# Optimization experiments

Measured on AMD Instinct MI355X. Metric: run time of the kernel, lower is better.

The kernel has to match this reference:

```python
import jax, jax.numpy as jnp
import numpy as np
import math

B, C, H, W = 16, 512, 32, 32
GROUPS = 32
EPS = 1e-5


def group_norm(x, w, b):
    # x: [B, C, H, W]; normalize within each of GROUPS channel groups over (C//G, H, W)
    Bx, Cx, Hx, Wx = x.shape
    xg = x.reshape(Bx, GROUPS, Cx // GROUPS, Hx, Wx)
    mean = xg.mean(axis=(2, 3, 4), keepdims=True)
    var = xg.var(axis=(2, 3, 4), keepdims=True)
    xg = (xg - mean) * jax.lax.rsqrt(var + EPS)
    xn = xg.reshape(Bx, Cx, Hx, Wx)
    return xn * w[None, :, None, None] + b[None, :, None, None]


def setup_inputs() -> dict:
    key = jax.random.key(0)
    ks = jax.random.split(key, 4)
    x = jax.random.normal(ks[0], (B, C, H, W), dtype=jnp.float32)
    gn_w = jnp.ones((C,), dtype=jnp.float32)
    gn_b = jnp.zeros((C,), dtype=jnp.float32)
    # Conv2d 1x1 weights as [out, in] matrices; PyTorch default init scale
    qkv_w = jax.random.normal(ks[1], (3 * C, C), dtype=jnp.float32) * (1.0 / math.sqrt(C))
    qkv_b = jnp.zeros((3 * C,), dtype=jnp.float32)
    out_w = jax.random.normal(ks[2], (C, C), dtype=jnp.float32) * (1.0 / math.sqrt(C))
    out_b = jnp.zeros((C,), dtype=jnp.float32)
    return {"x": x, "gn_w": gn_w, "gn_b": gn_b, "qkv_w": qkv_w,
            "qkv_b": qkv_b, "out_w": out_w, "out_b": out_b}


def reference(x, gn_w, gn_b, qkv_w, qkv_b, out_w, out_b):
    Bx, Cx, Hx, Wx = x.shape
    N = Hx * Wx
    h = group_norm(x, gn_w, gn_b)                       # [B, C, H, W]
    hf = h.reshape(Bx, Cx, N)                           # [B, C, N]
    # 1x1 conv == channel matmul
    qkv = jnp.einsum('oc,bcn->bon', qkv_w, hf) + qkv_b[None, :, None]  # [B, 3C, N]
    q, k, v = jnp.split(qkv, 3, axis=1)                 # each [B, C, N]
    q = q.transpose(0, 2, 1)                            # [B, N, C]
    v = v.transpose(0, 2, 1)                            # [B, N, C]
    scale = 1.0 / math.sqrt(Cx)
    attn = jnp.einsum('bnc,bcm->bnm', q, k) * scale     # [B, N, N]
    attn = jax.nn.softmax(attn, axis=-1)
    o = jnp.einsum('bnm,bmc->bnc', attn, v)             # [B, N, C]
    o = o.transpose(0, 2, 1)                            # [B, C, N]
    o = jnp.einsum('oc,bcn->bon', out_w, o) + out_b[None, :, None]
    return x + o.reshape(Bx, Cx, Hx, Wx)
```

## Files before the change

kernel.cpp:

```cpp
#include <hip/hip_runtime.h>

typedef unsigned short u16;
typedef short short8 __attribute__((ext_vector_type(8)));
typedef float floatx4 __attribute__((ext_vector_type(4)));
typedef u16 u16x4 __attribute__((ext_vector_type(4)));
typedef u16 u16x8 __attribute__((ext_vector_type(8)));

#define DEVI __device__ __forceinline__

DEVI u16 f2bf(float x) {
    union { float f; unsigned u; } c; c.f = x;
    unsigned u = c.u;
    u += 0x7fffu + ((u >> 16) & 1u);
    return (u16)(u >> 16);
}
DEVI float bf2f(u16 h) {
    union { unsigned u; float f; } c; c.u = ((unsigned)h) << 16;
    return c.f;
}

DEVI void gload_lds16(const void* g, void* l) {
    auto gp = (const __attribute__((address_space(1))) unsigned*)(unsigned long long)g;
    auto lp = (__attribute__((address_space(3))) unsigned*)(unsigned)(unsigned long long)l;
    __builtin_amdgcn_global_load_lds(gp, lp, 16, 0, 0);
}

__global__ __launch_bounds__(256) void gn_fused_kernel(const float* __restrict__ x,
                                                       const float* __restrict__ w,
                                                       const float* __restrict__ bb,
                                                       u16* __restrict__ h) {
    const int bg = blockIdx.x;
    const int b = bg >> 5, g = bg & 31;
    const float* xg = x + (long long)bg * 16384;
    const int n0 = threadIdx.x * 4;

    float4 xv[16];
    float s = 0.f, s2 = 0.f;
    #pragma unroll
    for (int cc = 0; cc < 16; cc++) {
        xv[cc] = *(const float4*)&xg[cc * 1024 + n0];
        s  += xv[cc].x + xv[cc].y + xv[cc].z + xv[cc].w;
        s2 += xv[cc].x*xv[cc].x + xv[cc].y*xv[cc].y + xv[cc].z*xv[cc].z + xv[cc].w*xv[cc].w;
    }
    #pragma unroll
    for (int m = 1; m < 64; m <<= 1) { s += __shfl_xor(s, m, 64); s2 += __shfl_xor(s2, m, 64); }
    __shared__ float rs[4], rq[4];
    if ((threadIdx.x & 63) == 0) { rs[threadIdx.x >> 6] = s; rq[threadIdx.x >> 6] = s2; }
    __syncthreads();
    float mean = (rs[0] + rs[1] + rs[2] + rs[3]) * (1.f / 16384.f);
    float var  = (rq[0] + rq[1] + rq[2] + rq[3]) * (1.f / 16384.f) - mean * mean;
    float rstd = rsqrtf(var + 1e-5f);

    u16x8 o[4][2];
    #pragma unroll
    for (int cc = 0; cc < 16; cc++) {
        int c = g * 16 + cc;
        float sc = w[c] * rstd;
        float sh = bb[c] - mean * sc;
        o[0][cc >> 3][cc & 7] = f2bf(xv[cc].x * sc + sh);
        o[1][cc >> 3][cc & 7] = f2bf(xv[cc].y * sc + sh);
        o[2][cc >> 3][cc & 7] = f2bf(xv[cc].z * sc + sh);
        o[3][cc >> 3][cc & 7] = f2bf(xv[cc].w * sc + sh);
    }
    u16* hb = h + ((long long)b * 1024 + n0) * 512 + g * 16;
    #pragma unroll
    for (int k = 0; k < 4; k++) {
        *(u16x8*)&hb[(long long)k * 512]     = o[k][0];
        *(u16x8*)&hb[(long long)k * 512 + 8] = o[k][1];
    }
}

__global__ __launch_bounds__(256) void wconv_kernel(const float* __restrict__ w1, u16* __restrict__ o1,
                                                    const float* __restrict__ w2, u16* __restrict__ o2) {
    int i = blockIdx.x * 256 + threadIdx.x;
    const float* src; u16* dst; int j;
    if (i < 196608) { src = w1; dst = o1; j = i; }
    else            { src = w2; dst = o2; j = i - 196608; }
    float4 v = *(const float4*)&src[j * 4];
    u16x4 p; p[0] = f2bf(v.x); p[1] = f2bf(v.y); p[2] = f2bf(v.z); p[3] = f2bf(v.w);
    *(u16x4*)&dst[j * 4] = p;
}

__global__ __launch_bounds__(256) void lreduce_kernel(const float* __restrict__ ps,
                                                      float* __restrict__ invl) {
    int i = blockIdx.x * 256 + threadIdx.x;
    int z = i >> 10, n = i & 1023;
    float l = 0.f;
    #pragma unroll
    for (int kb = 0; kb < 4; kb++) l += ps[((z * 4 + kb) << 10) + n];
    invl[i] = 1.f / l;
}

#define VMCNT(N) do { asm volatile("s_waitcnt vmcnt(" #N ")" ::: "memory"); \
                      __builtin_amdgcn_sched_barrier(0); } while (0)

template <bool EXPSTATS, bool AFFINE>
__global__ __launch_bounds__(512, 2)
void gemm256_kernel(const u16* __restrict__ A, const u16* __restrict__ Bt,
                    u16* __restrict__ C, float* __restrict__ aux,
                    float scale, int lda, int ldb, int ldc,
                    long long sA, long long sB, long long sC, int K) {
    int bx, by, bz;
    if (AFFINE) {
        const int lid = blockIdx.x;
        const int slot = lid >> 3;
        bz = (lid & 7) + 8 * (slot >> 4);
        const int w = slot & 15;
        bx = w & 3; by = w >> 2;
    } else { bx = blockIdx.x; by = blockIdx.y; bz = 0; }

    const int t    = threadIdx.x;
    const int lane = t & 63;
    const int wave = t >> 6;
    const int wm   = wave >> 2;
    const int wn   = wave & 3;
    const int quad = lane >> 4, lrow = lane & 15;
    const int m0 = by * 256, n0 = bx * 256;

    __shared__ __align__(16) u16 smem[65536];

    const int NT = K >> 6;

    floatx4 acc[8][4];
    #pragma unroll
    for (int i = 0; i < 8; i++)
        #pragma unroll
        for (int j = 0; j < 4; j++)
            #pragma unroll
            for (int r = 0; r < 4; r++) acc[i][j][r] = 0.f;

    const int srow = t >> 3;
    const int koff = ((t & 7) * 8) ^ (((t >> 5) & 1) << 4);
    const u16* Ab = A  + (long long)bz * sA + (long long)(m0 + srow) * lda + koff;
    const u16* Bb = Bt + (long long)bz * sB + (long long)(n0 + srow) * ldb + koff;

#define STGA(BUF, HALF, KT) do { \
    const u16* gs_ = Ab + (long long)((HALF) * 128) * lda + (KT) * 64; \
    gload_lds16(gs_,                          smem + ((BUF)*2 + (HALF)) * 8192 + t * 8); \
    gload_lds16(gs_ + (long long)64 * lda,    smem + ((BUF)*2 + (HALF)) * 8192 + 4096 + t * 8); \
} while (0)
#define STGB(BUF, HALF, KT) do { \
    const u16* gs_ = Bb + (long long)((HALF) * 128) * ldb + (KT) * 64; \
    gload_lds16(gs_,                          smem + 32768 + ((BUF)*2 + (HALF)) * 8192 + t * 8); \
    gload_lds16(gs_ + (long long)64 * ldb,    smem + 32768 + ((BUF)*2 + (HALF)) * 8192 + 4096 + t * 8); \
} while (0)

    const int swz  = ((lrow >> 2) & 1) << 4;
    const int arow = wm * 64 + lrow;
    const int brow = wn * 32 + lrow;
#define AIDX(BUF, QA, i, kk) (((BUF)*2 + (QA)) * 8192 + ((((arow + (i)*16) << 6) + (kk)*32 + (quad << 3)) ^ swz))
#define BIDX(BUF, QB, j, kk) (32768 + ((BUF)*2 + (QB)) * 8192 + ((((brow + (j)*16) << 6) + (kk)*32 + (quad << 3)) ^ swz))

#define PHASE(BUF, QA, QB, STG_STMT) do { \
    short8 paf[4][2], pbf[2][2]; \
    _Pragma("unroll") for (int i = 0; i < 4; ++i) { \
        paf[i][0] = *(const short8*)&smem[AIDX(BUF, QA, i, 0)]; \
        paf[i][1] = *(const short8*)&smem[AIDX(BUF, QA, i, 1)]; } \
    _Pragma("unroll") for (int j = 0; j < 2; ++j) { \
        pbf[j][0] = *(const short8*)&smem[BIDX(BUF, QB, j, 0)]; \
        pbf[j][1] = *(const short8*)&smem[BIDX(BUF, QB, j, 1)]; } \
    STG_STMT; \
    __builtin_amdgcn_s_barrier(); \
    __builtin_amdgcn_s_setprio(1); \
    _Pragma("unroll") for (int i = 0; i < 4; ++i) \
        _Pragma("unroll") for (int j = 0; j < 2; ++j) { \
            acc[(QA)*4 + i][(QB)*2 + j] = __builtin_amdgcn_mfma_f32_16x16x32_bf16( \
                paf[i][0], pbf[j][0], acc[(QA)*4 + i][(QB)*2 + j], 0, 0, 0); \
            acc[(QA)*4 + i][(QB)*2 + j] = __builtin_amdgcn_mfma_f32_16x16x32_bf16( \
                paf[i][1], pbf[j][1], acc[(QA)*4 + i][(QB)*2 + j], 0, 0, 0); } \
    __builtin_amdgcn_s_setprio(0); \
    __builtin_amdgcn_s_barrier(); \
} while (0)

    STGA(0, 0, 0); STGA(0, 1, 0); STGB(0, 0, 0); STGB(0, 1, 0);
    STGA(1, 0, 1); STGB(1, 0, 1);
    asm volatile("s_waitcnt vmcnt(0)" ::: "memory");
    __builtin_amdgcn_s_barrier();

    for (int tau = 0; tau < NT - 1; ++tau) {
        const int buf = tau & 1, nbuf = buf ^ 1;
        const bool s2 = tau < NT - 2;
        VMCNT(8); PHASE(buf, 0, 0, { STGA(nbuf, 1, tau + 1); });
        VMCNT(8); PHASE(buf, 1, 0, { STGB(nbuf, 1, tau + 1); });
        VMCNT(8); PHASE(buf, 0, 1, { if (s2) STGB(buf, 0, tau + 2); });
                  PHASE(buf, 1, 1, { if (s2) STGA(buf, 0, tau + 2); });
    }
    {
        const int buf = (NT - 1) & 1;
        VMCNT(4); PHASE(buf, 0, 0, {});
        VMCNT(2); PHASE(buf, 1, 0, {});
        VMCNT(0); PHASE(buf, 0, 1, {});
                  PHASE(buf, 1, 1, {});
    }

    const int ST2 = 272;
    const int erow = t >> 3;
    const int ec0  = (t & 7) * 32;
    #pragma unroll
    for (int s = 0; s < 4; ++s) {
        if (s) __syncthreads();
        if (wm == (s & 1)) {
            const int qa = s >> 1;
            #pragma unroll
            for (int i = 0; i < 4; ++i)
                #pragma unroll
                for (int cf = 0; cf < 4; ++cf) {
                    const int col = (cf >> 1) * 128 + wn * 32 + (cf & 1) * 16 + lrow;
                    #pragma unroll
                    for (int r = 0; r < 4; ++r) {
                        float v = acc[qa * 4 + i][cf][r] * scale;
                        if (EXPSTATS) v = __expf(v);
                        smem[(i * 16 + quad * 4 + r) * ST2 + col] = f2bf(v);
                    }
                }
        }
        __syncthreads();
        u16x8 y[4];
        #pragma unroll
        for (int kq = 0; kq < 4; ++kq) y[kq] = *(u16x8*)&smem[erow * ST2 + ec0 + kq * 8];
        u16* Cp = C + (long long)bz * sC + (long long)(m0 + s * 64 + erow) * ldc + n0 + ec0;
        #pragma unroll
        for (int kq = 0; kq < 4; ++kq) *(u16x8*)(Cp + kq * 8) = y[kq];
        if (EXPSTATS) {
            float ls = 0.f;
            #pragma unroll
            for (int kq = 0; kq < 4; ++kq)
                #pragma unroll
                for (int e = 0; e < 8; ++e) ls += bf2f(y[kq][e]);
            ls += __shfl_xor(ls, 1, 64);
            ls += __shfl_xor(ls, 2, 64);
            ls += __shfl_xor(ls, 4, 64);
            if ((t & 7) == 0)
                aux[((long long)(bz * 4 + bx)) * 1024 + m0 + s * 64 + erow] = ls;
        }
    }
#undef STGA
#undef STGB
#undef AIDX
#undef BIDX
#undef PHASE
}

template <int MODE, int NX, int NY, bool STATS>
__global__ __launch_bounds__(256, 3)
void gemm_bt_kernel(const u16* __restrict__ A, const u16* __restrict__ Bt,
                    void* __restrict__ C0,
                    const float* __restrict__ bias, const float* __restrict__ res,
                    float* __restrict__ aux,
                    float scale, int lda, int ldb, int ldc,
                    long long sA, long long sB, long long sC, long long sR, int K) {
    int bx, by, bz;
    if (NX > 0) {
        const int lid  = blockIdx.x;
        const int xcd  = lid & 7;
        const int slot = lid >> 3;
        const int per  = NX * NY;
        const int j    = slot / per;
        const int w    = slot - j * per;
        bz = xcd + 8 * j;
        bx = w % NX;
        by = w / NX;
    } else {
        bx = blockIdx.x; by = blockIdx.y; bz = blockIdx.z;
    }
    const int t    = threadIdx.x;
    const int lane = t & 63;
    const int wave = t >> 6;
    const int m0   = by * 128;
    const int n0   = bx * 128;
    A  += (long long)bz * sA;
    Bt += (long long)bz * sB;

    __shared__ __align__(16) u16 smem[16384];
    u16* As = smem;
    u16* Bs = smem + 8192;

    const int wm = wave >> 1, wn = wave & 1;
    const int quad = lane >> 4, lrow = lane & 15;

    floatx4 acc[4][4];
    #pragma unroll
    for (int i = 0; i < 4; i++)
        #pragma unroll
        for (int j = 0; j < 4; j++)
            #pragma unroll
            for (int r = 0; r < 4; r++) acc[i][j][r] = 0.f;

    const int rowA = t >> 2;
    const int kch  = (t & 3) * 8;
    const u16* Ag = A  + (long long)(m0 + rowA) * lda + kch;
    const u16* Bg = Bt + (long long)(n0 + rowA) * ldb + kch;
    u16* Al = &As[t * 8];
    u16* Bl = &Bs[t * 8];
    const long long a64 = (long long)64 * lda;
    const long long b64 = (long long)64 * ldb;

    for (int k0 = 0; k0 < K; k0 += 64) {
        gload_lds16(Ag + k0,            Al);
        gload_lds16(Ag + k0 + a64,      Al + 2048);
        gload_lds16(Ag + k0 + 32,       Al + 4096);
        gload_lds16(Ag + k0 + 32 + a64, Al + 6144);
        gload_lds16(Bg + k0,            Bl);
        gload_lds16(Bg + k0 + b64,      Bl + 2048);
        gload_lds16(Bg + k0 + 32,       Bl + 4096);
        gload_lds16(Bg + k0 + 32 + b64, Bl + 6144);
        __syncthreads();
        #pragma unroll
        for (int kk = 0; kk < 2; kk++) {
            short8 af[4], bfr[4];
            #pragma unroll
            for (int i = 0; i < 4; i++)
                af[i] = *(const short8*)&As[kk*4096 + (wm*64 + i*16 + lrow)*32 + quad*8];
            #pragma unroll
            for (int j = 0; j < 4; j++)
                bfr[j] = *(const short8*)&Bs[kk*4096 + (wn*64 + j*16 + lrow)*32 + quad*8];
            #pragma unroll
            for (int i = 0; i < 4; i++)
                #pragma unroll
                for (int j = 0; j < 4; j++)
                    acc[i][j] = __builtin_amdgcn_mfma_f32_16x16x32_bf16(af[i], bfr[j], acc[i][j], 0, 0, 0);
        }
        __syncthreads();
    }

    const int ST = 136;

    if (MODE == 2) {
        #pragma unroll
        for (int p = 0; p < 4; p++) {
            if (p) __syncthreads();
            if (wn == (p >> 1)) {
                #pragma unroll
                for (int jj = 0; jj < 2; jj++) {
                    const int j = (p & 1) * 2 + jj;
                    const int row = jj * 16 + lrow;
                    #pragma unroll
                    for (int i = 0; i < 4; i++) {
                        const int mmL = wm * 64 + i * 16 + quad * 4;
                        u16x4 pk;
                        #pragma unroll
                        for (int r = 0; r < 4; r++)
                            pk[r] = f2bf(acc[i][j][r] + bias[m0 + mmL + r]);
                        *(u16x4*)&smem[row * ST + mmL] = pk;
                    }
                }
            }
            __syncthreads();
            const int rr = t >> 3, cc = (t & 7) * 16;
            u16x8 a0 = *(u16x8*)&smem[rr * ST + cc];
            u16x8 a1 = *(u16x8*)&smem[rr * ST + cc + 8];
            u16* Cp = (u16*)C0 + (long long)(n0 + p * 32 + rr) * ldc + m0 + cc;
            *(u16x8*)Cp = a0;
            *(u16x8*)(Cp + 8) = a1;
        }
    } else {
        float* smf = (float*)smem;
        const int SF = 132;
        float* C = (float*)C0 + (long long)bz * sC;
        const float* rz = res + (long long)bz * sR;
        const float* il = aux + (long long)bz * 1024;
        #pragma unroll
        for (int p = 0; p < 8; p++) {
            if (p) __syncthreads();
            if (wm == (p >> 2)) {
                const int i = p & 3;
                #pragma unroll
                for (int j = 0; j < 4; j++) {
                    const int cB = wn * 64 + j * 16 + lrow;
                    #pragma unroll
                    for (int r = 0; r < 4; r++)
                        smf[(quad * 4 + r) * SF + cB] = acc[i][j][r];
                }
            }
            __syncthreads();
            const int rr = t >> 4, cc = (t & 15) * 8;
            const float bsv = bias[m0 + p * 16 + rr];
            float4 il0 = *(const float4*)&il[n0 + cc];
            float4 il1 = *(const float4*)&il[n0 + cc + 4];
            const long long gro = (long long)(m0 + p * 16 + rr) * ldc + n0 + cc;
            float4 rv0 = *(const float4*)&rz[gro];
            float4 rv1 = *(const float4*)&rz[gro + 4];
            float4 ov0, ov1;
            ov0.x = smf[rr*SF + cc + 0] * il0.x + bsv + rv0.x;
            ov0.y = smf[rr*SF + cc + 1] * il0.y + bsv + rv0.y;
            ov0.z = smf[rr*SF + cc + 2] * il0.z + bsv + rv0.z;
            ov0.w = smf[rr*SF + cc + 3] * il0.w + bsv + rv0.w;
            ov1.x = smf[rr*SF + cc + 4] * il1.x + bsv + rv1.x;
            ov1.y = smf[rr*SF + cc + 5] * il1.y + bsv + rv1.y;
            ov1.z = smf[rr*SF + cc + 6] * il1.z + bsv + rv1.z;
            ov1.w = smf[rr*SF + cc + 7] * il1.w + bsv + rv1.w;
            *(float4*)&C[gro]     = ov0;
            *(float4*)&C[gro + 4] = ov1;
        }
    }
}

extern "C" void kernel_launch(void* const* d_in, const int* in_sizes, int n_in,
                              void* d_out, int out_size, void* d_ws, size_t ws_size,
                              hipStream_t stream) {
    (void)in_sizes; (void)n_in; (void)out_size; (void)ws_size;
    const float* x     = (const float*)d_in[0];
    const float* gn_w  = (const float*)d_in[1];
    const float* gn_b  = (const float*)d_in[2];
    const float* qkv_w = (const float*)d_in[3];
    const float* qkv_b = (const float*)d_in[4];
    const float* out_w = (const float*)d_in[5];
    const float* out_b = (const float*)d_in[6];
    float* out = (float*)d_out;

    char* ws = (char*)d_ws;
    u16*  h_t   = (u16*)ws;  ws += (size_t)16*1024*512*2;
    u16*  qkv_t = (u16*)ws;  ws += (size_t)16*1024*1536*2;
    u16*  vprm  = (u16*)ws;  ws += (size_t)512*16384*2;
    u16*  E     = (u16*)ws;  ws += (size_t)16*1024*1024*2;
    u16*  wq    = (u16*)ws;  ws += (size_t)1536*512*2;
    u16*  wo    = (u16*)ws;  ws += (size_t)512*512*2;
    float* psum = (float*)ws; ws += (size_t)16*8*1024*4;
    float* invl = (float*)ws; ws += (size_t)16*1024*4;

    wconv_kernel<<<1024, 256, 0, stream>>>(qkv_w, wq, out_w, wo);
    gn_fused_kernel<<<512, 256, 0, stream>>>(x, gn_w, gn_b, h_t);

    gemm_bt_kernel<2, 0, 0, false><<<dim3(128, 12, 1), 256, 0, stream>>>(
        wq, h_t, qkv_t, qkv_b, nullptr, nullptr, 1.0f,
        512, 512, 1536, 0, 0, 0, 0, 512);

    gemm256_kernel<false, false><<<dim3(64, 2, 1), 512, 0, stream>>>(
        wo, qkv_t + 1024, vprm, nullptr, 1.0f,
        512, 1536, 16384, 0, 0, 0, 512);

    gemm256_kernel<true, true><<<256, 512, 0, stream>>>(
        qkv_t, qkv_t + 512, E, psum, 0.044194173824159216f,
        1536, 1536, 1024,
        (long long)1024*1536, (long long)1024*1536, (long long)1024*1024, 512);

    lreduce_kernel<<<64, 256, 0, stream>>>(psum, invl);

    gemm_bt_kernel<3, 8, 4, false><<<512, 256, 0, stream>>>(
        vprm, E, out, out_b, x, invl, 1.0f,
        16384, 1024, 1024,
        1024, (long long)1024*1024, (long long)512*1024, (long long)512*1024, 1024);
}
```

Baseline: 229.7 us.

## Restructure 256-tile GEMM main loop with K-split LDS layout and B-fragment reuse

Reorganizes the 256x256 bf16 GEMM's inner loop. The LDS layout is now split into two 32-wide K halves with a new XOR swizzle, and B fragments are held across sub-phases (pb0/pb1) so each B quarter is read from LDS once per K-tile instead of twice. Explicit lgkmcnt waits and barriers are placed between the fragment loads and the MFMA blocks. Launch bounds drop to one block of 512 threads per CU, freeing registers for the extra fragments at the cost of occupancy. The other GEMM template gains a minimum-waves parameter that keeps its current default.

After: 218.3 us. -5.0%, faster.

```diff
diff --git a/kernel.cpp b/kernel.cpp
--- a/kernel.cpp
+++ b/kernel.cpp
@@ -93,9 +93,12 @@
 
 #define VMCNT(N) do { asm volatile("s_waitcnt vmcnt(" #N ")" ::: "memory"); \
                       __builtin_amdgcn_sched_barrier(0); } while (0)
+#define LGKM0 do { asm volatile("s_waitcnt lgkmcnt(0)" ::: "memory"); \
+                   __builtin_amdgcn_sched_barrier(0); } while (0)
+#define BAR __builtin_amdgcn_s_barrier()
 
 template <bool EXPSTATS, bool AFFINE>
-__global__ __launch_bounds__(512, 2)
+__global__ __launch_bounds__(512, 1)
 void gemm256_kernel(const u16* __restrict__ A, const u16* __restrict__ Bt,
                     u16* __restrict__ C, float* __restrict__ aux,
                     float scale, int lda, int ldb, int ldc,
@@ -129,68 +132,76 @@
             #pragma unroll
             for (int r = 0; r < 4; r++) acc[i][j][r] = 0.f;
 
-    const int srow = t >> 3;
-    const int koff = ((t & 7) * 8) ^ (((t >> 5) & 1) << 4);
-    const u16* Ab = A  + (long long)bz * sA + (long long)(m0 + srow) * lda + koff;
-    const u16* Bb = Bt + (long long)bz * sB + (long long)(n0 + srow) * ldb + koff;
+    const int srow  = t >> 2;
+    const int skoff = ((t & 3) * 8) ^ ((((t >> 3)) & 3) << 3);
+    const u16* Ab = A  + (long long)bz * sA + (long long)(m0 + srow) * lda + skoff;
+    const u16* Bb = Bt + (long long)bz * sB + (long long)(n0 + srow) * ldb + skoff;
 
 #define STGA(BUF, HALF, KT) do { \
-    const u16* gs_ = Ab + (long long)((HALF) * 128) * lda + (KT) * 64; \
-    gload_lds16(gs_,                          smem + ((BUF)*2 + (HALF)) * 8192 + t * 8); \
-    gload_lds16(gs_ + (long long)64 * lda,    smem + ((BUF)*2 + (HALF)) * 8192 + 4096 + t * 8); \
+    const u16* g_ = Ab + (long long)((HALF) * 128) * lda + (KT) * 64; \
+    gload_lds16(g_,      smem + ((BUF)*2 + (HALF)) * 8192 + t * 8); \
+    gload_lds16(g_ + 32, smem + ((BUF)*2 + (HALF)) * 8192 + 4096 + t * 8); \
 } while (0)
 #define STGB(BUF, HALF, KT) do { \
-    const u16* gs_ = Bb + (long long)((HALF) * 128) * ldb + (KT) * 64; \
-    gload_lds16(gs_,                          smem + 32768 + ((BUF)*2 + (HALF)) * 8192 + t * 8); \
-    gload_lds16(gs_ + (long long)64 * ldb,    smem + 32768 + ((BUF)*2 + (HALF)) * 8192 + 4096 + t * 8); \
+    const u16* g_ = Bb + (long long)((HALF) * 128) * ldb + (KT) * 64; \
+    gload_lds16(g_,      smem + 32768 + ((BUF)*2 + (HALF)) * 8192 + t * 8); \
+    gload_lds16(g_ + 32, smem + 32768 + ((BUF)*2 + (HALF)) * 8192 + 4096 + t * 8); \
 } while (0)
 
-    const int swz  = ((lrow >> 2) & 1) << 4;
+    const int rswz = (lrow >> 1) & 3;
     const int arow = wm * 64 + lrow;
     const int brow = wn * 32 + lrow;
-#define AIDX(BUF, QA, i, kk) (((BUF)*2 + (QA)) * 8192 + ((((arow + (i)*16) << 6) + (kk)*32 + (quad << 3)) ^ swz))
-#define BIDX(BUF, QB, j, kk) (32768 + ((BUF)*2 + (QB)) * 8192 + ((((brow + (j)*16) << 6) + (kk)*32 + (quad << 3)) ^ swz))
-
-#define PHASE(BUF, QA, QB, STG_STMT) do { \
-    short8 paf[4][2], pbf[2][2]; \
-    _Pragma("unroll") for (int i = 0; i < 4; ++i) { \
-        paf[i][0] = *(const short8*)&smem[AIDX(BUF, QA, i, 0)]; \
-        paf[i][1] = *(const short8*)&smem[AIDX(BUF, QA, i, 1)]; } \
-    _Pragma("unroll") for (int j = 0; j < 2; ++j) { \
-        pbf[j][0] = *(const short8*)&smem[BIDX(BUF, QB, j, 0)]; \
-        pbf[j][1] = *(const short8*)&smem[BIDX(BUF, QB, j, 1)]; } \
-    STG_STMT; \
-    __builtin_amdgcn_s_barrier(); \
-    __builtin_amdgcn_s_setprio(1); \
+#define AIDX(BUF, QA, i, kk) (((BUF)*2 + (QA)) * 8192 + (kk) * 4096 + (arow + (i)*16) * 32 + ((quad ^ rswz) << 3))
+#define BIDX(BUF, QB, j, kk) (32768 + ((BUF)*2 + (QB)) * 8192 + (kk) * 4096 + (brow + (j)*16) * 32 + ((quad ^ rswz) << 3))
+
+    short8 pa[4][2], pb0[2][2], pb1[2][2];
+#define LOADA(BUF, QA) do { _Pragma("unroll") for (int i = 0; i < 4; ++i) { \
+    pa[i][0] = *(const short8*)&smem[AIDX(BUF, QA, i, 0)]; \
+    pa[i][1] = *(const short8*)&smem[AIDX(BUF, QA, i, 1)]; } } while (0)
+#define LOADB(BUF, QB, PB) do { _Pragma("unroll") for (int j = 0; j < 2; ++j) { \
+    PB[j][0] = *(const short8*)&smem[BIDX(BUF, QB, j, 0)]; \
+    PB[j][1] = *(const short8*)&smem[BIDX(BUF, QB, j, 1)]; } } while (0)
+#define MM(QA, QB, PB) do { __builtin_amdgcn_s_setprio(1); \
     _Pragma("unroll") for (int i = 0; i < 4; ++i) \
         _Pragma("unroll") for (int j = 0; j < 2; ++j) { \
             acc[(QA)*4 + i][(QB)*2 + j] = __builtin_amdgcn_mfma_f32_16x16x32_bf16( \
-                paf[i][0], pbf[j][0], acc[(QA)*4 + i][(QB)*2 + j], 0, 0, 0); \
+                pa[i][0], PB[j][0], acc[(QA)*4 + i][(QB)*2 + j], 0, 0, 0); \
             acc[(QA)*4 + i][(QB)*2 + j] = __builtin_amdgcn_mfma_f32_16x16x32_bf16( \
-                paf[i][1], pbf[j][1], acc[(QA)*4 + i][(QB)*2 + j], 0, 0, 0); } \
-    __builtin_amdgcn_s_setprio(0); \
-    __builtin_amdgcn_s_barrier(); \
-} while (0)
-
-    STGA(0, 0, 0); STGA(0, 1, 0); STGB(0, 0, 0); STGB(0, 1, 0);
+                pa[i][1], PB[j][1], acc[(QA)*4 + i][(QB)*2 + j], 0, 0, 0); } \
+    __builtin_amdgcn_s_setprio(0); } while (0)
+
+    STGA(0, 0, 0); STGB(0, 0, 0); STGA(0, 1, 0); STGB(0, 1, 0);
+    asm volatile("s_waitcnt vmcnt(0)" ::: "memory");
+    BAR;
     STGA(1, 0, 1); STGB(1, 0, 1);
-    asm volatile("s_waitcnt vmcnt(0)" ::: "memory");
-    __builtin_amdgcn_s_barrier();
 
     for (int tau = 0; tau < NT - 1; ++tau) {
         const int buf = tau & 1, nbuf = buf ^ 1;
         const bool s2 = tau < NT - 2;
-        VMCNT(8); PHASE(buf, 0, 0, { STGA(nbuf, 1, tau + 1); });
-        VMCNT(8); PHASE(buf, 1, 0, { STGB(nbuf, 1, tau + 1); });
-        VMCNT(8); PHASE(buf, 0, 1, { if (s2) STGB(buf, 0, tau + 2); });
-                  PHASE(buf, 1, 1, { if (s2) STGA(buf, 0, tau + 2); });
+        VMCNT(8);
+        LOADA(buf, 0); LOADB(buf, 0, pb0);
+        STGA(nbuf, 1, tau + 1);
+        BAR; LGKM0; MM(0, 0, pb0); BAR;
+        VMCNT(6);
+        LOADB(buf, 1, pb1);
+        STGB(nbuf, 1, tau + 1);
+        BAR; LGKM0; MM(0, 1, pb1); BAR;
+        LOADA(buf, 1);
+        if (s2) { STGA(buf, 0, tau + 2); STGB(buf, 0, tau + 2); }
+        BAR; LGKM0; MM(1, 0, pb0); BAR;
+        MM(1, 1, pb1);
     }
     {
         const int buf = (NT - 1) & 1;
-        VMCNT(4); PHASE(buf, 0, 0, {});
-        VMCNT(2); PHASE(buf, 1, 0, {});
-        VMCNT(0); PHASE(buf, 0, 1, {});
-                  PHASE(buf, 1, 1, {});
+        VMCNT(4);
+        LOADA(buf, 0); LOADB(buf, 0, pb0);
+        BAR; LGKM0; MM(0, 0, pb0); BAR;
+        VMCNT(0);
+        LOADB(buf, 1, pb1);
+        BAR; LGKM0; MM(0, 1, pb1); BAR;
+        LOADA(buf, 1);
+        BAR; LGKM0; MM(1, 0, pb0); BAR;
+        MM(1, 1, pb1);
     }
 
     const int ST2 = 272;
@@ -238,11 +249,13 @@
 #undef STGB
 #undef AIDX
 #undef BIDX
-#undef PHASE
-}
-
-template <int MODE, int NX, int NY, bool STATS>
-__global__ __launch_bounds__(256, 3)
+#undef LOADA
+#undef LOADB
+#undef MM
+}
+
+template <int MODE, int NX, int NY, bool STATS, int MINW = 3>
+__global__ __launch_bounds__(256, MINW)
 void gemm_bt_kernel(const u16* __restrict__ A, const u16* __restrict__ Bt,
                     void* __restrict__ C0,
                     const float* __restrict__ bias, const float* __restrict__ res,
@@ -421,7 +434,7 @@
     wconv_kernel<<<1024, 256, 0, stream>>>(qkv_w, wq, out_w, wo);
     gn_fused_kernel<<<512, 256, 0, stream>>>(x, gn_w, gn_b, h_t);
 
-    gemm_bt_kernel<2, 0, 0, false><<<dim3(128, 12, 1), 256, 0, stream>>>(
+    gemm_bt_kernel<2, 0, 0, false, 3><<<dim3(128, 12, 1), 256, 0, stream>>>(
         wq, h_t, qkv_t, qkv_b, nullptr, nullptr, 1.0f,
         512, 512, 1536, 0, 0, 0, 0, 512);
 
@@ -436,7 +449,7 @@
 
     lreduce_kernel<<<64, 256, 0, stream>>>(psum, invl);
 
-    gemm_bt_kernel<3, 8, 4, false><<<512, 256, 0, stream>>>(
+    gemm_bt_kernel<3, 8, 4, false, 3><<<512, 256, 0, stream>>>(
         vprm, E, out, out_b, x, invl, 1.0f,
         16384, 1024, 1024,
         1024, (long long)1024*1024, (long long)512*1024, (long long)512*1024, 1024);
```
